# Kernel tuning notes

Hardware: AMD Instinct MI355X
Metric: run time of the kernel (lower is better)

## Reference

```python
import jax, jax.numpy as jnp
import numpy as np

B, CLN, QL, IH, IW = 64, 32, 32, 16, 16
CDF, SL = 256, 128
IDF = CLN * IH * IW  # 8192


def setup_inputs() -> dict:
    key = jax.random.key(0)
    k1, k2, k3 = jax.random.split(key, 3)
    inp = jax.random.normal(k1, (B, CLN, QL, IH, IW), dtype=jnp.float32)
    context = jax.random.normal(k2, (B, CDF, SL), dtype=jnp.float32)
    # Conv2d(cdf, idf, 1, bias=False) weight, squeezed to [idf, cdf]
    W = jax.random.normal(k3, (IDF, CDF), dtype=jnp.float32) * (1.0 / np.sqrt(CDF))
    return {"input": inp, "context": context, "W": W}


def reference(input, context, W):
    b, cln, queryL, ih, iw = input.shape
    idf = cln * ih * iw
    sourceL = context.shape[2]
    # target: b x queryL x (cln*ih*iw)
    targetT = jnp.transpose(input, (0, 2, 1, 3, 4)).reshape(b, queryL, idf)
    # 1x1 conv projection of context: b x idf x sourceL
    sourceT = jnp.einsum('oc,bcs->bos', W, context)
    # attention scores and softmax over sourceL (nn.Softmax on 2D -> dim=1)
    attn = jnp.einsum('bqd,bds->bqs', targetT, sourceT)  # b x queryL x sourceL
    attn = jax.nn.softmax(attn, axis=-1)
    attnT = jnp.transpose(attn, (0, 2, 1))  # b x sourceL x queryL
    # weighted context: b x idf x queryL
    wc = jnp.einsum('bds,bsq->bdq', sourceT, attnT)
    # faithful to torch .view: raw row-major reinterpretation of [b, idf, queryL]
    wc = wc.reshape(b, queryL, cln, ih, iw)
    wc = jnp.transpose(wc, (0, 2, 1, 3, 4))  # b x cln x queryL x ih x iw
    return (wc, attnT)
```

## Files before the change

### kernel.cpp

```cpp
#include <hip/hip_runtime.h>
#include <math.h>


#define ZK 16

typedef _Float16 f16x8 __attribute__((ext_vector_type(8)));
typedef float f32x4 __attribute__((ext_vector_type(4)));

#define GLDS16(gp, lp)                                                          \
    __builtin_amdgcn_global_load_lds(                                           \
        (const __attribute__((address_space(1))) void*)(gp),                    \
        (__attribute__((address_space(3))) void*)(lp), 16, 0, 0)

__global__ __launch_bounds__(256) void k0a_prep(const float* __restrict__ Wm,
                                                _Float16* __restrict__ Wth,
                                                _Float16* __restrict__ Wtl) {
    const int kb = blockIdx.x;
    const int t = threadIdx.x;
    __shared__ float tile[32][260];
    {
        const int r = t >> 3;
        const int c0 = (t & 7) * 32;
        const float* src = Wm + (long)(kb * 32 + r) * 256 + c0;
#pragma unroll
        for (int i = 0; i < 8; ++i) {
            float4 v = *(const float4*)(src + i * 4);
            tile[r][c0 + i * 4 + 0] = v.x;
            tile[r][c0 + i * 4 + 1] = v.y;
            tile[r][c0 + i * 4 + 2] = v.z;
            tile[r][c0 + i * 4 + 3] = v.w;
        }
    }
    __syncthreads();
    const int lane = t & 63;
    const int quad = lane >> 4, l15 = lane & 15;
#pragma unroll
    for (int i = 0; i < 4; ++i) {
        int nsub = (t >> 6) * 4 + i;
        f16x8 oh, ol;
#pragma unroll
        for (int j = 0; j < 8; ++j) {
            float f = tile[quad * 8 + j][nsub * 16 + l15];
            _Float16 h = (_Float16)f;
            oh[j] = h;
            ol[j] = (_Float16)(f - (float)h);
        }
        long addr = ((long)(kb * 16 + nsub) * 64 + lane) * 8;
        *(f16x8*)(Wth + addr) = oh;
        *(f16x8*)(Wtl + addr) = ol;
    }
}

__global__ __launch_bounds__(256) void k0b_prep(const float* __restrict__ Wm,
                                                _Float16* __restrict__ Wbf) {
    const int t = threadIdx.x;
    const int fid = blockIdx.x * 4 + (t >> 6);
    const int mb = fid >> 3, kb4 = fid & 7;
    const int lane = t & 63;
    const int quad = lane >> 4, l15 = lane & 15;
    const float* src = Wm + (long)(mb * 16 + l15) * 256 + kb4 * 32 + quad * 8;
    float4 u0 = *(const float4*)(src);
    float4 u1 = *(const float4*)(src + 4);
    f16x8 o;
    o[0] = (_Float16)u0.x; o[1] = (_Float16)u0.y;
    o[2] = (_Float16)u0.z; o[3] = (_Float16)u0.w;
    o[4] = (_Float16)u1.x; o[5] = (_Float16)u1.y;
    o[6] = (_Float16)u1.z; o[7] = (_Float16)u1.w;
    *(f16x8*)(Wbf + ((long)fid * 64 + lane) * 8) = o;
}

__global__ __launch_bounds__(512, 2) void k1_mfma(const float* __restrict__ inp,
                                                  const _Float16* __restrict__ Wth,
                                                  const _Float16* __restrict__ Wtl,
                                                  float* __restrict__ tWpart) {
    const int m0 = blockIdx.x * 128;
    const int kz = blockIdx.y;
    const int t = threadIdx.x;
    const int lane = t & 63, wv = t >> 6;
    const int quad = lane >> 4, l15 = lane & 15;
    const int mi = wv >> 2;
    const int ni = wv & 3;

    __shared__ float As[2][128][32];

    const int srow = t >> 3;
    const int swc = ((t & 7) ^ (srow & 7)) * 4;
    const float* sb0;
    const float* sb1;
    {
        int mA = m0 + srow;
        sb0 = inp + (long)(mA >> 5) * 262144 + (long)(mA & 31) * 256 + swc;
        mA = m0 + 64 + srow;
        sb1 = inp + (long)(mA >> 5) * 262144 + (long)(mA & 31) * 256 + swc;
    }
    float* lbase0 = &As[0][0][0] + wv * 256;
    float* lbase1 = &As[0][64][0] + wv * 256;
    float* lbase0b = &As[1][0][0] + wv * 256;
    float* lbase1b = &As[1][64][0] + wv * 256;

    f32x4 acc[4][4];
#pragma unroll
    for (int i = 0; i < 4; ++i)
#pragma unroll
        for (int j = 0; j < 4; ++j) acc[i][j] = (f32x4){0.f, 0.f, 0.f, 0.f};

    f16x8 Bh[2][4], Bl[2][4];

    {
        const int k0g = kz * 512;
        const long o = (long)(k0g >> 8) * 8192 + (k0g & 255);
        GLDS16(sb0 + o, lbase0);
        GLDS16(sb1 + o, lbase1);
        const long bb = ((long)((kz * 16) * 16 + ni * 4) * 64 + lane) * 8;
#pragma unroll
        for (int j = 0; j < 4; ++j) {
            Bh[0][j] = *(const f16x8*)(Wth + bb + (long)j * 512);
            Bl[0][j] = *(const f16x8*)(Wtl + bb + (long)j * 512);
        }
    }

#pragma unroll
    for (int it = 0; it < 16; ++it) {
        const int cur = it & 1, nxt = cur ^ 1;
        if (it < 15) {
            const int k0g = kz * 512 + (it + 1) * 32;
            const long o = (long)(k0g >> 8) * 8192 + (k0g & 255);
            if (nxt) { GLDS16(sb0 + o, lbase0b); GLDS16(sb1 + o, lbase1b); }
            else     { GLDS16(sb0 + o, lbase0);  GLDS16(sb1 + o, lbase1);  }
            const long bb = ((long)((kz * 16 + it + 1) * 16 + ni * 4) * 64 + lane) * 8;
#pragma unroll
            for (int j = 0; j < 4; ++j) {
                Bh[nxt][j] = *(const f16x8*)(Wth + bb + (long)j * 512);
                Bl[nxt][j] = *(const f16x8*)(Wtl + bb + (long)j * 512);
            }
        }
        __builtin_amdgcn_sched_barrier(0);
        if (it < 15) asm volatile("s_waitcnt vmcnt(10)" ::: "memory");
        else         asm volatile("s_waitcnt vmcnt(0)" ::: "memory");
        __builtin_amdgcn_sched_barrier(0);
        __builtin_amdgcn_s_barrier();

        f16x8 ah[4], al[4];
#pragma unroll
        for (int i = 0; i < 4; ++i) {
            const int row = (mi * 4 + i) * 16 + l15;
            const int x = row & 7;
            float4 f0 = *(const float4*)&As[cur][row][((quad * 2) ^ x) * 4];
            float4 f1 = *(const float4*)&As[cur][row][((quad * 2 + 1) ^ x) * 4];
            float ff[8] = {f0.x, f0.y, f0.z, f0.w, f1.x, f1.y, f1.z, f1.w};
#pragma unroll
            for (int j = 0; j < 8; ++j) {
                _Float16 h = (_Float16)ff[j];
                ah[i][j] = h;
                al[i][j] = (_Float16)(ff[j] - (float)h);
            }
        }
        asm volatile("s_waitcnt lgkmcnt(0)" ::: "memory");
        __builtin_amdgcn_sched_barrier(0);
        __builtin_amdgcn_s_barrier();

#pragma unroll
        for (int i = 0; i < 4; ++i)
#pragma unroll
            for (int j = 0; j < 4; ++j) {
                acc[i][j] = __builtin_amdgcn_mfma_f32_16x16x32_f16(ah[i], Bh[cur][j], acc[i][j], 0, 0, 0);
                acc[i][j] = __builtin_amdgcn_mfma_f32_16x16x32_f16(al[i], Bh[cur][j], acc[i][j], 0, 0, 0);
                acc[i][j] = __builtin_amdgcn_mfma_f32_16x16x32_f16(ah[i], Bl[cur][j], acc[i][j], 0, 0, 0);
            }
    }

    float* outp = tWpart + (long)kz * 524288;
#pragma unroll
    for (int i = 0; i < 4; ++i) {
        const int mbase = m0 + (mi * 4 + i) * 16 + quad * 4;
#pragma unroll
        for (int j = 0; j < 4; ++j) {
            const int c = (ni * 4 + j) * 16 + l15;
#pragma unroll
            for (int rg = 0; rg < 4; ++rg)
                outp[(long)(mbase + rg) * 256 + c] = acc[i][j][rg];
        }
    }
}

__global__ __launch_bounds__(256) void k2_logits_softmax(const float* __restrict__ tWpart,
                                                         const float* __restrict__ ctx,
                                                         float* __restrict__ attnT) {
    const int qg = blockIdx.x;
    const int b  = blockIdx.y;
    const int t  = threadIdx.x;
    __shared__ float tw4[4][256];
#pragma unroll
    for (int qq = 0; qq < 4; ++qq) {
        const float* p = tWpart + (long)(b * 32 + qg * 4 + qq) * 256 + t;
        float s = 0.f;
#pragma unroll
        for (int z = 0; z < ZK; ++z) s += p[(long)z * 524288];
        tw4[qq][t] = s;
    }
    __syncthreads();
    const int q = t >> 6, lane = t & 63;
    const float* ctxb = ctx + (long)b * 32768 + lane * 2;
    float ax = 0.f, ay = 0.f;
#pragma unroll 4
    for (int c = 0; c < 256; ++c) {
        float tw = tw4[q][c];
        float2 cv = *(const float2*)(ctxb + c * 128);
        ax = fmaf(tw, cv.x, ax);
        ay = fmaf(tw, cv.y, ay);
    }
    float mx = fmaxf(ax, ay);
#pragma unroll
    for (int m = 1; m <= 32; m <<= 1) mx = fmaxf(mx, __shfl_xor(mx, m));
    float ex = expf(ax - mx);
    float ey = expf(ay - mx);
    float sm = ex + ey;
#pragma unroll
    for (int m = 1; m <= 32; m <<= 1) sm += __shfl_xor(sm, m);
    float inv = 1.f / sm;
    ex *= inv; ey *= inv;
    float* o = attnT + (long)b * 4096 + (qg * 4 + q);
    o[(lane * 2 + 0) * 32] = ex;
    o[(lane * 2 + 1) * 32] = ey;
}

__global__ __launch_bounds__(256) void k3_ctxA(const float* __restrict__ ctx,
                                               const float* __restrict__ attnT,
                                               _Float16* __restrict__ ctxAqf) {
    const int cg = blockIdx.x;
    const int b  = blockIdx.y;
    const int t  = threadIdx.x;
    __shared__ float at[128][32];
    __shared__ float cs[32][132];
#pragma unroll
    for (int i = 0; i < 4; ++i)
        *(float4*)((float*)at + i * 1024 + t * 4) =
            *(const float4*)(attnT + (long)b * 4096 + i * 1024 + t * 4);
#pragma unroll
    for (int i = 0; i < 4; ++i) {
        int idx = i * 256 + t;
        int c = idx >> 5, sseg = (idx & 31) * 4;
        *(float4*)&cs[c][sseg] = *(const float4*)(ctx + (long)b * 32768 + (long)(cg * 32 + c) * 128 + sseg);
    }
    __syncthreads();
    const int c = t >> 3;
    const int qs = (t & 7) * 4;
    float4 acc = make_float4(0.f, 0.f, 0.f, 0.f);
#pragma unroll 4
    for (int s = 0; s < 128; ++s) {
        float cv = cs[c][s];
        float4 av = *(const float4*)&at[s][qs];
        acc.x = fmaf(cv, av.x, acc.x);
        acc.y = fmaf(cv, av.y, acc.y);
        acc.z = fmaf(cv, av.z, acc.z);
        acc.w = fmaf(cv, av.w, acc.w);
    }
    const int cglob = cg * 32 + c;
    const long cpart = (long)(cglob >> 5) * 64 + 16 * ((cglob >> 3) & 3);
    float vals[4] = {acc.x, acc.y, acc.z, acc.w};
#pragma unroll
    for (int u = 0; u < 4; ++u) {
        int n = b * 32 + qs + u;
        long addr = ((long)(n >> 4) * 8 * 64 + cpart + (n & 15)) * 8 + (cglob & 7);
        ctxAqf[addr] = (_Float16)vals[u];
    }
}

__global__ __launch_bounds__(256) void k4_mfma(const _Float16* __restrict__ Wbf,
                                               const _Float16* __restrict__ ctxAqf,
                                               float* __restrict__ out0) {
    const int t = threadIdx.x;
    const int lane = t & 63, wv = t >> 6;
    const int mb = blockIdx.x * 4 + wv;
    const int nb0 = blockIdx.y * 8;
    const _Float16* abase = Wbf + ((long)mb * 8 * 64 + lane) * 8;
    const _Float16* bbase = ctxAqf + ((long)nb0 * 8 * 64 + lane) * 8;

    f32x4 acc[8];
#pragma unroll
    for (int j = 0; j < 8; ++j) acc[j] = (f32x4){0.f, 0.f, 0.f, 0.f};

#pragma unroll
    for (int kb = 0; kb < 8; ++kb) {
        f16x8 af = *(const f16x8*)(abase + (long)kb * 512);
#pragma unroll
        for (int j = 0; j < 8; ++j) {
            f16x8 bf = *(const f16x8*)(bbase + (long)(j * 8 + kb) * 512);
            acc[j] = __builtin_amdgcn_mfma_f32_16x16x32_f16(af, bf, acc[j], 0, 0, 0);
        }
    }
    const int quad = lane >> 4, col = lane & 15;
#pragma unroll
    for (int j = 0; j < 8; ++j) {
        const int n = (nb0 + j) * 16 + col;
        float* ob = out0 + (long)(n >> 5) * 262144 + (n & 31);
#pragma unroll
        for (int rg = 0; rg < 4; ++rg) {
            const int d = mb * 16 + quad * 4 + rg;
            ob[(long)((d >> 3) & 31) * 8192 + (long)(d >> 8) * 256 + (long)(d & 7) * 32] = acc[j][rg];
        }
    }
}

extern "C" void kernel_launch(void* const* d_in, const int* in_sizes, int n_in,
                              void* d_out, int out_size, void* d_ws, size_t ws_size,
                              hipStream_t stream) {
    const float* inp = (const float*)d_in[0];
    const float* ctx = (const float*)d_in[1];
    const float* Wm  = (const float*)d_in[2];
    float* out0 = (float*)d_out;
    float* out1 = out0 + 16777216;

    float* wsf = (float*)d_ws;
    float* tWpart = wsf;
    _Float16* Wbf    = (_Float16*)wsf;
    _Float16* ctxAqf = (_Float16*)(wsf + 1048576);
    _Float16* Wth = (_Float16*)(wsf + 8388608);
    _Float16* Wtl = Wth + 2097152;

    hipLaunchKernelGGL(k0a_prep, dim3(256), dim3(256), 0, stream, Wm, Wth, Wtl);
    hipLaunchKernelGGL(k1_mfma, dim3(16, ZK), dim3(512), 0, stream, inp, Wth, Wtl, tWpart);
    hipLaunchKernelGGL(k2_logits_softmax, dim3(8, 64), dim3(256), 0, stream, tWpart, ctx, out1);
    hipLaunchKernelGGL(k0b_prep, dim3(1024), dim3(256), 0, stream, Wm, Wbf);
    hipLaunchKernelGGL(k3_ctxA, dim3(8, 64), dim3(256), 0, stream, ctx, out1, ctxAqf);
    hipLaunchKernelGGL(k4_mfma, dim3(128, 16), dim3(256), 0, stream, Wbf, ctxAqf, out0);
}
```

Before: 219.6 us.

## Triple-buffer k1 A tiles with one barrier per step, stage k4 B in LDS

In k1, the LDS A-tile ring goes from two buffers to three, so loads are issued two steps ahead and each k-step needs only one barrier instead of two. The block index is also remapped so that consecutive blocks cover different k-splits of the same m tile, which changes L2 locality. In k4, each block first stages its shared context B fragments into LDS with direct global-to-LDS loads, so the four waves no longer each fetch them from global memory. The trade-off is more LDS per block (48KB in k1, 64KB in k4), which may lower occupancy, and the vmcnt(10) wait count must still match the new number of loads in flight.

```diff
diff --git a/kernel.cpp b/kernel.cpp
--- a/kernel.cpp
+++ b/kernel.cpp
@@ -73,15 +73,16 @@
                                                   const _Float16* __restrict__ Wth,
                                                   const _Float16* __restrict__ Wtl,
                                                   float* __restrict__ tWpart) {
-    const int m0 = blockIdx.x * 128;
-    const int kz = blockIdx.y;
+    const int lin = blockIdx.x + (blockIdx.y << 4);
+    const int kz = lin & 15;
+    const int m0 = (lin >> 4) * 128;
     const int t = threadIdx.x;
     const int lane = t & 63, wv = t >> 6;
     const int quad = lane >> 4, l15 = lane & 15;
     const int mi = wv >> 2;
     const int ni = wv & 3;
 
-    __shared__ float As[2][128][32];
+    __shared__ float As[3][128][32];
 
     const int srow = t >> 3;
     const int swc = ((t & 7) ^ (srow & 7)) * 4;
@@ -93,10 +94,6 @@
         mA = m0 + 64 + srow;
         sb1 = inp + (long)(mA >> 5) * 262144 + (long)(mA & 31) * 256 + swc;
     }
-    float* lbase0 = &As[0][0][0] + wv * 256;
-    float* lbase1 = &As[0][64][0] + wv * 256;
-    float* lbase0b = &As[1][0][0] + wv * 256;
-    float* lbase1b = &As[1][64][0] + wv * 256;
 
     f32x4 acc[4][4];
 #pragma unroll
@@ -107,10 +104,13 @@
     f16x8 Bh[2][4], Bl[2][4];
 
     {
-        const int k0g = kz * 512;
-        const long o = (long)(k0g >> 8) * 8192 + (k0g & 255);
-        GLDS16(sb0 + o, lbase0);
-        GLDS16(sb1 + o, lbase1);
+        long o = (long)((kz * 512) >> 8) * 8192 + ((kz * 512) & 255);
+        GLDS16(sb0 + o, &As[0][0][0] + wv * 256);
+        GLDS16(sb1 + o, &As[0][64][0] + wv * 256);
+        const int k1g = kz * 512 + 32;
+        o = (long)(k1g >> 8) * 8192 + (k1g & 255);
+        GLDS16(sb0 + o, &As[1][0][0] + wv * 256);
+        GLDS16(sb1 + o, &As[1][64][0] + wv * 256);
         const long bb = ((long)((kz * 16) * 16 + ni * 4) * 64 + lane) * 8;
 #pragma unroll
         for (int j = 0; j < 4; ++j) {
@@ -122,11 +122,19 @@
 #pragma unroll
     for (int it = 0; it < 16; ++it) {
         const int cur = it & 1, nxt = cur ^ 1;
+        if (it < 15) asm volatile("s_waitcnt vmcnt(10)" ::: "memory");
+        else         asm volatile("s_waitcnt vmcnt(0)" ::: "memory");
+        __builtin_amdgcn_sched_barrier(0);
+        __builtin_amdgcn_s_barrier();
+        __builtin_amdgcn_sched_barrier(0);
+
+        if (it < 14) {
+            const int kg = kz * 512 + (it + 2) * 32;
+            const long o = (long)(kg >> 8) * 8192 + (kg & 255);
+            GLDS16(sb0 + o, &As[(it + 2) % 3][0][0] + wv * 256);
+            GLDS16(sb1 + o, &As[(it + 2) % 3][64][0] + wv * 256);
+        }
         if (it < 15) {
-            const int k0g = kz * 512 + (it + 1) * 32;
-            const long o = (long)(k0g >> 8) * 8192 + (k0g & 255);
-            if (nxt) { GLDS16(sb0 + o, lbase0b); GLDS16(sb1 + o, lbase1b); }
-            else     { GLDS16(sb0 + o, lbase0);  GLDS16(sb1 + o, lbase1);  }
             const long bb = ((long)((kz * 16 + it + 1) * 16 + ni * 4) * 64 + lane) * 8;
 #pragma unroll
             for (int j = 0; j < 4; ++j) {
@@ -135,18 +143,14 @@
             }
         }
         __builtin_amdgcn_sched_barrier(0);
-        if (it < 15) asm volatile("s_waitcnt vmcnt(10)" ::: "memory");
-        else         asm volatile("s_waitcnt vmcnt(0)" ::: "memory");
-        __builtin_amdgcn_sched_barrier(0);
-        __builtin_amdgcn_s_barrier();
 
         f16x8 ah[4], al[4];
 #pragma unroll
         for (int i = 0; i < 4; ++i) {
             const int row = (mi * 4 + i) * 16 + l15;
             const int x = row & 7;
-            float4 f0 = *(const float4*)&As[cur][row][((quad * 2) ^ x) * 4];
-            float4 f1 = *(const float4*)&As[cur][row][((quad * 2 + 1) ^ x) * 4];
+            float4 f0 = *(const float4*)&As[it % 3][row][((quad * 2) ^ x) * 4];
+            float4 f1 = *(const float4*)&As[it % 3][row][((quad * 2 + 1) ^ x) * 4];
             float ff[8] = {f0.x, f0.y, f0.z, f0.w, f1.x, f1.y, f1.z, f1.w};
 #pragma unroll
             for (int j = 0; j < 8; ++j) {
@@ -155,9 +159,6 @@
                 al[i][j] = (_Float16)(ff[j] - (float)h);
             }
         }
-        asm volatile("s_waitcnt lgkmcnt(0)" ::: "memory");
-        __builtin_amdgcn_sched_barrier(0);
-        __builtin_amdgcn_s_barrier();
 
 #pragma unroll
         for (int i = 0; i < 4; ++i)
@@ -273,8 +274,20 @@
     const int lane = t & 63, wv = t >> 6;
     const int mb = blockIdx.x * 4 + wv;
     const int nb0 = blockIdx.y * 8;
+
+    __shared__ _Float16 Bs[32768];
+
+    {
+        const _Float16* gsrc = ctxAqf + (long)nb0 * 4096;
+#pragma unroll
+        for (int i = 0; i < 16; ++i) {
+            const int chunk = i * 256 + wv * 64;
+            GLDS16(gsrc + (long)chunk * 8 + lane * 8, Bs + chunk * 8);
+        }
+    }
+    __syncthreads();
+
     const _Float16* abase = Wbf + ((long)mb * 8 * 64 + lane) * 8;
-    const _Float16* bbase = ctxAqf + ((long)nb0 * 8 * 64 + lane) * 8;
 
     f32x4 acc[8];
 #pragma unroll
@@ -285,7 +298,7 @@
         f16x8 af = *(const f16x8*)(abase + (long)kb * 512);
 #pragma unroll
         for (int j = 0; j < 8; ++j) {
-            f16x8 bf = *(const f16x8*)(bbase + (long)(j * 8 + kb) * 512);
+            f16x8 bf = *(const f16x8*)(Bs + (j * 8 + kb) * 512 + lane * 8);
             acc[j] = __builtin_amdgcn_mfma_f32_16x16x32_f16(af, bf, acc[j], 0, 0, 0);
         }
     }
```

Measured after the change: 218.2 us. About the same (-0.6%).
